# Kernel optimization log

Hardware: AMD Instinct MI355X
Metric: run time of the kernel (lower is better)

Reference implementation:

```python
import jax, jax.numpy as jnp
import numpy as np

B, S_IMG, S_TXT, D, H, HD = 1, 2048, 512, 3072, 24, 128
EMB, N_IP = 4096, 64
IP_SCALE = 1.0
EPS = 1e-6
SM_SCALE = 1.0 / np.sqrt(HD).astype(np.float32)


def _lin(x, W, b=None):
    # torch Linear: y = x @ W.T + b, W: [out, in]
    y = jnp.einsum('bsd,od->bso', x, W)
    return y if b is None else y + b


def _heads(x):  # [B,S,D] -> [B,H,S,HD]
    return x.reshape(B, -1, H, HD).transpose(0, 2, 1, 3)


def _rms(x, w):
    return x * jax.lax.rsqrt(jnp.mean(x * x, axis=-1, keepdims=True) + EPS) * w


def _rope(x, cos, sin):
    # interleaved real/imag rotation, cos/sin: [S, HD] broadcast over B,H
    xr = x.reshape(*x.shape[:-1], HD // 2, 2)
    rot = jnp.stack([-xr[..., 1], xr[..., 0]], axis=-1).reshape(x.shape)
    return x * cos + rot * sin


def _sdpa(q, k, v):
    s = jnp.einsum('bhqd,bhkd->bhqk', q, k) * SM_SCALE
    p = jax.nn.softmax(s, axis=-1)
    return jnp.einsum('bhqk,bhkd->bhqd', p, v)


def setup_inputs() -> dict:
    key = jax.random.key(0)
    ks = jax.random.split(key, 32)
    r = lambda i, shape: jax.random.normal(ks[i], shape, dtype=jnp.float32)
    w = lambda i, shape: r(i, shape) * 0.02
    inp = {
        'hidden_states': r(0, (B, S_IMG, D)),
        'encoder_hidden_states': r(1, (B, S_TXT, D)),
        'image_embeds': r(2, (B, N_IP, EMB)),
        'rope_cos': jnp.cos(r(3, (S_TXT + S_IMG, HD))),
        'rope_sin': jnp.sin(r(3, (S_TXT + S_IMG, HD))),
        'Wq': w(4, (D, D)), 'bq': jnp.zeros((D,)),
        'Wk': w(5, (D, D)), 'bk': jnp.zeros((D,)),
        'Wv': w(6, (D, D)), 'bv': jnp.zeros((D,)),
        'Waq': w(7, (D, D)), 'baq': jnp.zeros((D,)),
        'Wak': w(8, (D, D)), 'bak': jnp.zeros((D,)),
        'Wav': w(9, (D, D)), 'bav': jnp.zeros((D,)),
        'Wo': w(10, (D, D)), 'bo': jnp.zeros((D,)),
        'Wao': w(11, (D, D)), 'bao': jnp.zeros((D,)),
        'norm_q_w': jnp.ones((HD,)), 'norm_k_w': jnp.ones((HD,)),
        'norm_aq_w': jnp.ones((HD,)), 'norm_ak_w': jnp.ones((HD,)),
        'Wk_ip': w(12, (D, EMB)), 'Wv_ip': w(13, (D, EMB)),
        'txt_seq_len': S_TXT,
    }
    return inp


def reference(hidden_states, encoder_hidden_states, image_embeds, rope_cos, rope_sin,
              Wq, bq, Wk, bk, Wv, bv, Waq, baq, Wak, bak, Wav, bav,
              Wo, bo, Wao, bao, norm_q_w, norm_k_w, norm_aq_w, norm_ak_w,
              Wk_ip, Wv_ip, txt_seq_len):
    # main stream projections + per-head RMSNorm
    q = _rms(_heads(_lin(hidden_states, Wq, bq)), norm_q_w)
    k = _rms(_heads(_lin(hidden_states, Wk, bk)), norm_k_w)
    v = _heads(_lin(hidden_states, Wv, bv))
    # encoder (text) stream projections + RMSNorm, concat text before image
    eq = _rms(_heads(_lin(encoder_hidden_states, Waq, baq)), norm_aq_w)
    ek = _rms(_heads(_lin(encoder_hidden_states, Wak, bak)), norm_ak_w)
    ev = _heads(_lin(encoder_hidden_states, Wav, bav))
    q = jnp.concatenate([eq, q], axis=2)
    k = jnp.concatenate([ek, k], axis=2)
    v = jnp.concatenate([ev, v], axis=2)
    # IP-adapter branch uses pre-RoPE image-token queries
    ip_q = q[:, :, txt_seq_len:]
    ip_k = _heads(_lin(image_embeds, Wk_ip))
    ip_v = _heads(_lin(image_embeds, Wv_ip))
    ip_hs = _sdpa(ip_q, ip_k, ip_v).transpose(0, 2, 1, 3).reshape(B, -1, H * HD)
    # rotary on joint q/k, then main attention
    q = _rope(q, rope_cos, rope_sin)
    k = _rope(k, rope_cos, rope_sin)
    hs = _sdpa(q, k, v).transpose(0, 2, 1, 3).reshape(B, -1, H * HD)
    # add scaled IP-adapter output to the image part
    img = hs[:, txt_seq_len:] + IP_SCALE * ip_hs
    enc = hs[:, :txt_seq_len]
    # output projections
    out_img = _lin(img, Wo, bo)
    out_enc = _lin(enc, Wao, bao)
    return out_img, out_enc
```

## Files before the change

kernel.cpp:

```cpp
#include <hip/hip_runtime.h>
#include <hip/hip_bf16.h>

#define H 24
#define HD 128
#define DMODEL 3072
#define S_IMG 2048
#define S_TXT 512
#define S_ALL 2560
#define EMB 4096
#define N_IP 64
#define SM_SCALE 0.08838834764831845f

typedef __attribute__((ext_vector_type(8))) short short8;
typedef __attribute__((ext_vector_type(4))) float f32x4;
typedef __attribute__((ext_vector_type(16))) float f32x16;

__device__ inline unsigned short f2bf(float f) {
    unsigned u = __builtin_bit_cast(unsigned, f);
    return (unsigned short)((u + 0x7fffu + ((u >> 16) & 1u)) >> 16);
}
__device__ inline unsigned pk2(float a, float b) {
    return (unsigned)f2bf(a) | ((unsigned)f2bf(b) << 16);
}
__device__ inline float bf2f(unsigned short u) {
    unsigned x = ((unsigned)u) << 16;
    return __builtin_bit_cast(float, x);
}

__device__ inline void gload16(const void* g, void* l) {
    __builtin_amdgcn_global_load_lds(
        (const __attribute__((address_space(1))) unsigned int*)g,
        (__attribute__((address_space(3))) unsigned int*)(unsigned int)(unsigned long long)l,
        16, 0, 0);
}

struct CastSegs {
    const float* src[13];
    unsigned short* dst[13];
    int n8[13];
    int ntot8[13];
    int bstart[14];
};

__global__ __launch_bounds__(256)
void castall(CastSegs cs)
{
    int b = blockIdx.x, seg = 0;
    while (seg < 12 && b >= cs.bstart[seg + 1]) seg++;
    int nb = cs.bstart[seg + 1] - cs.bstart[seg];
    int lb = b - cs.bstart[seg];
    const float* in = cs.src[seg];
    unsigned short* out = cs.dst[seg];
    int n8 = cs.n8[seg], ntot = cs.ntot8[seg];
    for (int i = lb * 256 + threadIdx.x; i < ntot; i += nb * 256) {
        int4 o;
        if (i < n8) {
            const float4* p = (const float4*)(in + (size_t)i * 8);
            float4 a = p[0], bb = p[1];
            o.x = pk2(a.x, a.y); o.y = pk2(a.z, a.w);
            o.z = pk2(bb.x, bb.y); o.w = pk2(bb.z, bb.w);
        } else {
            o.x = 0; o.y = 0; o.z = 0; o.w = 0;
        }
        *(int4*)(out + (size_t)i * 8) = o;
    }
}

__global__ __launch_bounds__(256)
void bcat2(const float* __restrict__ q0, const float* __restrict__ k0, const float* __restrict__ v0,
           const float* __restrict__ q1, const float* __restrict__ k1, const float* __restrict__ v1,
           float* __restrict__ d0, float* __restrict__ d1)
{
    int i = blockIdx.x * 256 + threadIdx.x;
    int which = i >= 3 * DMODEL;
    int j = which ? i - 3 * DMODEL : i;
    const float* a = which ? q1 : q0;
    const float* b = which ? k1 : k0;
    const float* c = which ? v1 : v0;
    float v = (j < DMODEL) ? a[j] : ((j < 2 * DMODEL) ? b[j - DMODEL] : c[j - 2 * DMODEL]);
    (which ? d1 : d0)[j] = v;
}

struct GSet {
    const unsigned short* A;
    const unsigned short* B;
    const float* bias;
    void* C;
    int N, K, nbn;
};

template<int OUTBF>
__global__ __launch_bounds__(512, 4)
void gemm8(GSet s0, GSet s1, GSet s2, int e0, int e1, int e2,
           const float* cs0, unsigned short* cd0,
           const float* cs1, unsigned short* cd1, int cn8)
{
    __shared__ char sm[73728];
    const int tid = threadIdx.x, lane = tid & 63, wid = tid >> 6;
    const int wm = wid >> 1, wn = wid & 1;
    const int r15 = lane & 15, g = lane >> 4;

    int nwg = gridDim.x;
    int t0 = (blockIdx.x & 7) * (nwg >> 3) + (blockIdx.x >> 3);

    if (t0 >= e2) {
        int lb = t0 - e2;
        const float* src = (lb >> 6) ? cs1 : cs0;
        unsigned short* dst = (lb >> 6) ? cd1 : cd0;
        int b = lb & 63;
        for (int i = b * 512 + tid; i < cn8; i += 64 * 512) {
            const float4* p = (const float4*)(src + (size_t)i * 8);
            float4 a = p[0], bb = p[1];
            int4 o;
            o.x = pk2(a.x, a.y); o.y = pk2(a.z, a.w);
            o.z = pk2(bb.x, bb.y); o.w = pk2(bb.z, bb.w);
            *(int4*)(dst + (size_t)i * 8) = o;
        }
        return;
    }

    GSet S; int local;
    if (t0 < e0)      { S = s0; local = t0; }
    else if (t0 < e1) { S = s1; local = t0 - e0; }
    else              { S = s2; local = t0 - e1; }
    const int mb = local / S.nbn, nb = local - mb * S.nbn;
    const int m0 = mb * 256, n0 = nb * 128;
    const int K = S.K, N = S.N;
    const unsigned short* A = S.A;
    const unsigned short* B = S.B;
    const float* bias = S.bias;

    const int fA0 = tid, fA1 = 512 + tid;
    const int rA0 = fA0 >> 2, sA0 = fA0 & 3;
    const int rA1 = fA1 >> 2, sA1 = fA1 & 3;
    const int rB = tid >> 2, sB = tid & 3;
    const unsigned short* Asrc0 = A + (size_t)(m0 + rA0) * K + ((sA0 ^ ((rA0 >> 1) & 3)) << 3);
    const unsigned short* Asrc1 = A + (size_t)(m0 + rA1) * K + ((sA1 ^ ((rA1 >> 1) & 3)) << 3);
    const unsigned short* Bsrc  = B + (size_t)(n0 + rB) * K + ((sB ^ ((rB >> 1) & 3)) << 3);

    f32x4 acc[4][4];
    #pragma unroll
    for (int i = 0; i < 4; i++)
        #pragma unroll
        for (int j = 0; j < 4; j++)
            acc[i][j] = {0.f, 0.f, 0.f, 0.f};

    const int nt = K >> 5;

    auto STAGE = [&](int buf, int kt) {
        char* d = sm + buf * 24576;
        gload16(Asrc0 + (kt << 5), d + fA0 * 16);
        gload16(Asrc1 + (kt << 5), d + fA1 * 16);
        gload16(Bsrc  + (kt << 5), d + 16384 + tid * 16);
    };

    STAGE(0, 0);
    STAGE(1, 1);
    asm volatile("s_waitcnt vmcnt(3)" ::: "memory");
    __builtin_amdgcn_s_barrier();

    int cur = 0, nxt = 2;
    for (int t = 0; t < nt; t++) {
        if (t + 2 < nt) STAGE(nxt, t + 2);
        const char* As = sm + cur * 24576;
        const char* Bs = As + 16384;
        short8 bfr[4];
        #pragma unroll
        for (int ni = 0; ni < 4; ni++) {
            int brow = wn * 64 + ni * 16 + r15;
            bfr[ni] = *(const short8*)(Bs + brow * 64 + ((g ^ ((brow >> 1) & 3)) << 4));
        }
        __builtin_amdgcn_s_setprio(1);
        #pragma unroll
        for (int mi = 0; mi < 4; mi++) {
            int arow = wm * 64 + mi * 16 + r15;
            short8 af = *(const short8*)(As + arow * 64 + ((g ^ ((arow >> 1) & 3)) << 4));
            #pragma unroll
            for (int ni = 0; ni < 4; ni++)
                acc[mi][ni] = __builtin_amdgcn_mfma_f32_16x16x32_bf16(af, bfr[ni], acc[mi][ni], 0, 0, 0);
        }
        __builtin_amdgcn_s_setprio(0);
        if (t + 1 < nt) {
            if (t + 2 < nt) { asm volatile("s_waitcnt vmcnt(3)" ::: "memory"); }
            else            { asm volatile("s_waitcnt vmcnt(0)" ::: "memory"); }
            __builtin_amdgcn_s_barrier();
        }
        cur = (cur == 2) ? 0 : cur + 1;
        nxt = (nxt == 2) ? 0 : nxt + 1;
    }

    #pragma unroll
    for (int mi = 0; mi < 4; mi++) {
        #pragma unroll
        for (int ni = 0; ni < 4; ni++) {
            int col = n0 + wn * 64 + ni * 16 + r15;
            float bv = bias ? bias[col] : 0.f;
            #pragma unroll
            for (int r = 0; r < 4; r++) {
                int grow = m0 + wm * 64 + mi * 16 + g * 4 + r;
                float v = acc[mi][ni][r] + bv;
                if (OUTBF)
                    ((unsigned short*)S.C)[(size_t)grow * N + col] = f2bf(v);
                else
                    ((float*)S.C)[(size_t)grow * N + col] = v;
            }
        }
    }
}

__device__ inline void vtrans_body(const unsigned short* __restrict__ base, int stride,
                                   unsigned short* __restrict__ vt, int Stot,
                                   int s0, int h, unsigned short* lv, int tid)
{
    const unsigned short* src = base + (size_t)s0 * stride + h * HD;
    #pragma unroll
    for (int i = 0; i < 4; i++) {
        int slot = tid + 256 * i;
        int row = slot >> 4, c = slot & 15;
        int4 v = *(const int4*)(src + (size_t)row * stride + c * 8);
        unsigned* p = (unsigned*)(lv + row * 130 + c * 8);
        p[0] = (unsigned)v.x; p[1] = (unsigned)v.y; p[2] = (unsigned)v.z; p[3] = (unsigned)v.w;
    }
    __syncthreads();
    #pragma unroll
    for (int i = 0; i < 4; i++) {
        int slot = tid + 256 * i;
        int d = slot >> 3, c8 = slot & 7;
        unsigned w0 = lv[(c8 * 8 + 0) * 130 + d] | ((unsigned)lv[(c8 * 8 + 1) * 130 + d] << 16);
        unsigned w1 = lv[(c8 * 8 + 2) * 130 + d] | ((unsigned)lv[(c8 * 8 + 3) * 130 + d] << 16);
        unsigned w2 = lv[(c8 * 8 + 4) * 130 + d] | ((unsigned)lv[(c8 * 8 + 5) * 130 + d] << 16);
        unsigned w3 = lv[(c8 * 8 + 6) * 130 + d] | ((unsigned)lv[(c8 * 8 + 7) * 130 + d] << 16);
        int4 o = {(int)w0, (int)w1, (int)w2, (int)w3};
        *(int4*)(vt + (size_t)(h * HD + d) * Stot + s0 + c8 * 8) = o;
    }
}

__global__ __launch_bounds__(256)
void epilogue(const unsigned short* __restrict__ qkvb, const unsigned short* __restrict__ ipkvb,
              const float* __restrict__ nqw, const float* __restrict__ nkw,
              const float* __restrict__ naqw, const float* __restrict__ nakw,
              const float* __restrict__ cosb, const float* __restrict__ sinb,
              unsigned short* __restrict__ qb, unsigned short* __restrict__ kb,
              unsigned short* __restrict__ ipq,
              unsigned short* __restrict__ vtb, unsigned short* __restrict__ ipkb,
              unsigned short* __restrict__ ipvtb)
{
    __shared__ unsigned short lv[64 * 130];
    const int b = blockIdx.x;
    const int tid = threadIdx.x;

    if (b < 15360) {
        int wg = b * 4 + (tid >> 6);
        int lane = tid & 63;
        int s = wg / H, h = wg - s * H;
        const unsigned short* row = qkvb + (size_t)s * (3 * DMODEL);
        unsigned uq = *(const unsigned*)(row + h * HD + lane * 2);
        unsigned uk = *(const unsigned*)(row + DMODEL + h * HD + lane * 2);
        float q0 = bf2f((unsigned short)uq), q1 = bf2f((unsigned short)(uq >> 16));
        float k0 = bf2f((unsigned short)uk), k1 = bf2f((unsigned short)(uk >> 16));
        float sq = q0 * q0 + q1 * q1, sk = k0 * k0 + k1 * k1;
        #pragma unroll
        for (int off = 1; off < 64; off <<= 1) {
            sq += __shfl_xor(sq, off);
            sk += __shfl_xor(sk, off);
        }
        float rq = rsqrtf(sq * (1.f / HD) + 1e-6f) * SM_SCALE;
        float rk = rsqrtf(sk * (1.f / HD) + 1e-6f);
        const float* wq = (s < S_TXT) ? naqw : nqw;
        const float* wk = (s < S_TXT) ? nakw : nkw;
        float xq0 = q0 * rq * wq[lane * 2], xq1 = q1 * rq * wq[lane * 2 + 1];
        float xk0 = k0 * rk * wk[lane * 2], xk1 = k1 * rk * wk[lane * 2 + 1];
        if (s >= S_TXT)
            *(unsigned*)(ipq + (size_t)h * S_IMG * HD + (size_t)(s - S_TXT) * HD + lane * 2) = pk2(xq0, xq1);
        float c0 = cosb[s * HD + lane * 2], c1 = cosb[s * HD + lane * 2 + 1];
        float s0 = sinb[s * HD + lane * 2], s1 = sinb[s * HD + lane * 2 + 1];
        *(unsigned*)(qb + (size_t)h * S_ALL * HD + (size_t)s * HD + lane * 2) =
            pk2(xq0 * c0 - xq1 * s0, xq1 * c1 + xq0 * s1);
        *(unsigned*)(kb + (size_t)h * S_ALL * HD + (size_t)s * HD + lane * 2) =
            pk2(xk0 * c0 - xk1 * s0, xk1 * c1 + xk0 * s1);
    } else if (b < 16320) {
        int local = b - 15360;
        int bx = local % 40, h = local / 40;
        vtrans_body(qkvb + 2 * DMODEL, 3 * DMODEL, vtb, S_ALL, bx * 64, h, lv, tid);
    } else if (b < 16416) {
        int idx = (b - 16320) * 256 + tid;
        int s = idx / 384;
        int rem = idx - s * 384;
        int h = rem >> 4, d8 = rem & 15;
        int4 v = *(const int4*)(ipkvb + (size_t)s * (2 * DMODEL) + h * HD + d8 * 8);
        *(int4*)(ipkb + ((size_t)h * N_IP + s) * HD + d8 * 8) = v;
    } else {
        int h = b - 16416;
        vtrans_body(ipkvb + DMODEL, 2 * DMODEL, ipvtb, N_IP, 0, h, lv, tid);
    }
}

template<int MODE, int KVBLK, int NQB>
__global__ __launch_bounds__(512, 2)
void flash4(const unsigned short* __restrict__ Q, const unsigned short* __restrict__ Kb,
            const unsigned short* __restrict__ Vt, const unsigned short* __restrict__ ipb,
            unsigned short* __restrict__ Out, int Sq, int Skv)
{
    __shared__ char sm[66560];
    int bid = blockIdx.x;
    int gidx = (bid & 7) * (gridDim.x >> 3) + (bid >> 3);
    const int h = gidx / NQB;
    const int q0 = (gidx - h * NQB) * 256;
    const int tid = threadIdx.x, w = tid >> 6, lane = tid & 63;
    const int l31 = lane & 31, hi = lane >> 5;
    const int T2 = KVBLK / 32, K4 = KVBLK / 16, SLOTV = KVBLK / 8, NL = KVBLK / 32;
    const int VROWB = KVBLK * 2;

    const unsigned short* Qh = Q + ((size_t)h * Sq + q0 + w * 32 + l31) * HD + hi * 8;
    short8 qf[8];
    #pragma unroll
    for (int c = 0; c < 8; c++)
        qf[c] = *(const short8*)(Qh + c * 16);

    float m = -3.0e38f, lsum = 0.f;
    f32x16 o[4];
    #pragma unroll
    for (int dn = 0; dn < 4; dn++)
        #pragma unroll
        for (int r = 0; r < 16; r++) o[dn][r] = 0.f;

    const unsigned short* Kh = Kb + (size_t)h * Skv * HD;
    const unsigned short* Vth = Vt + (size_t)h * HD * Skv;
    float* scl = (float*)(sm + 65536) + w * 32;
    const int nt = Skv / KVBLK;

    for (int t = 0; t < nt; t++) {
        int kv0 = t * KVBLK;
        #pragma unroll
        for (int cc = 0; cc < NL; cc++) {
            int f = cc * 512 + tid;
            int row = f >> 4, slot = f & 15;
            gload16(Kh + (size_t)(kv0 + row) * HD + (((slot * 16) ^ ((row & 7) << 4)) >> 1),
                    sm + f * 16);
        }
        #pragma unroll
        for (int cc = 0; cc < NL; cc++) {
            int f = cc * 512 + tid;
            int d = f / SLOTV, slot = f % SLOTV;
            gload16(Vth + (size_t)d * Skv + kv0 + (((slot * 16) ^ ((d & 7) << 4)) >> 1),
                    sm + 32768 + f * 16);
        }
        __syncthreads();

        f32x16 st[T2];
        __builtin_amdgcn_s_setprio(1);
        #pragma unroll
        for (int t2 = 0; t2 < T2; t2++) {
            #pragma unroll
            for (int r = 0; r < 16; r++) st[t2][r] = 0.f;
            #pragma unroll
            for (int c = 0; c < 8; c++) {
                int krow = t2 * 32 + l31;
                short8 kf = *(const short8*)(sm + krow * 256 + ((c * 32 + hi * 16) ^ ((krow & 7) << 4)));
                st[t2] = __builtin_amdgcn_mfma_f32_32x32x16_bf16(kf, qf[c], st[t2], 0, 0, 0);
            }
        }
        __builtin_amdgcn_s_setprio(0);

        float pmax = st[0][0];
        #pragma unroll
        for (int t2 = 0; t2 < T2; t2++)
            #pragma unroll
            for (int r = 0; r < 16; r++) pmax = fmaxf(pmax, st[t2][r]);
        pmax = fmaxf(pmax, __shfl_xor(pmax, 32));

        if (!__all(pmax - m <= 8.0f)) {
            float mn = fmaxf(m, pmax);
            float sc = __expf(m - mn);
            m = mn;
            lsum *= sc;
            if (hi == 0) scl[l31] = sc;
            float scb[16];
            #pragma unroll
            for (int r = 0; r < 16; r++)
                scb[r] = scl[(r & 3) + 8 * (r >> 2) + 4 * hi];
            #pragma unroll
            for (int dn = 0; dn < 4; dn++)
                #pragma unroll
                for (int r = 0; r < 16; r++) o[dn][r] *= scb[r];
        }

        float psum = 0.f;
        #pragma unroll
        for (int t2 = 0; t2 < T2; t2++)
            #pragma unroll
            for (int r = 0; r < 16; r++) {
                float p = __expf(st[t2][r] - m);
                st[t2][r] = p;
                psum += p;
            }
        psum += __shfl_xor(psum, 32);
        lsum += psum;

        short8 pa[K4];
        #pragma unroll
        for (int k4 = 0; k4 < K4; k4++) {
            unsigned U  = pk2(st[(k4 * 8 + 0) >> 4][(k4 * 8 + 0) & 15], st[(k4 * 8 + 1) >> 4][(k4 * 8 + 1) & 15]);
            unsigned V  = pk2(st[(k4 * 8 + 2) >> 4][(k4 * 8 + 2) & 15], st[(k4 * 8 + 3) >> 4][(k4 * 8 + 3) & 15]);
            unsigned U2 = pk2(st[(k4 * 8 + 4) >> 4][(k4 * 8 + 4) & 15], st[(k4 * 8 + 5) >> 4][(k4 * 8 + 5) & 15]);
            unsigned V2 = pk2(st[(k4 * 8 + 6) >> 4][(k4 * 8 + 6) & 15], st[(k4 * 8 + 7) >> 4][(k4 * 8 + 7) & 15]);
            unsigned SU = __shfl_xor(U, 32), SU2 = __shfl_xor(U2, 32);
            unsigned SV = __shfl_xor(V, 32), SV2 = __shfl_xor(V2, 32);
            uint4 wv;
            wv.x = hi ? SU2 : U;
            wv.y = hi ? SV2 : V;
            wv.z = hi ? U2 : SU;
            wv.w = hi ? V2 : SV;
            pa[k4] = __builtin_bit_cast(short8, wv);
        }

        __builtin_amdgcn_s_setprio(1);
        #pragma unroll
        for (int dn = 0; dn < 4; dn++) {
            #pragma unroll
            for (int k4 = 0; k4 < K4; k4++) {
                int vrow = dn * 32 + l31;
                short8 vf = *(const short8*)(sm + 32768 + vrow * VROWB + ((k4 * 32 + hi * 16) ^ ((vrow & 7) << 4)));
                o[dn] = __builtin_amdgcn_mfma_f32_32x32x16_bf16(pa[k4], vf, o[dn], 0, 0, 0);
            }
        }
        __builtin_amdgcn_s_setprio(0);
        __syncthreads();
    }

    if (hi == 0) scl[l31] = 1.f / lsum;
    float linv[16];
    #pragma unroll
    for (int r = 0; r < 16; r++)
        linv[r] = scl[(r & 3) + 8 * (r >> 2) + 4 * hi];
    #pragma unroll
    for (int dn = 0; dn < 4; dn++) {
        #pragma unroll
        for (int r = 0; r < 16; r++) {
            int qrow = q0 + w * 32 + (r & 3) + 8 * (r >> 2) + 4 * hi;
            int col = h * HD + dn * 32 + l31;
            float val = o[dn][r] * linv[r];
            if (MODE == 1 && qrow >= S_TXT)
                val += bf2f(ipb[(size_t)(qrow - S_TXT) * DMODEL + col]);
            Out[(size_t)qrow * DMODEL + col] = f2bf(val);
        }
    }
}

extern "C" void kernel_launch(void* const* d_in, const int* in_sizes, int n_in,
                              void* d_out, int out_size, void* d_ws, size_t ws_size,
                              hipStream_t stream)
{
    const float* hs   = (const float*)d_in[0];
    const float* enc  = (const float*)d_in[1];
    const float* iemb = (const float*)d_in[2];
    const float* cosb = (const float*)d_in[3];
    const float* sinb = (const float*)d_in[4];
    const float* Wq  = (const float*)d_in[5];  const float* bq  = (const float*)d_in[6];
    const float* Wk  = (const float*)d_in[7];  const float* bk  = (const float*)d_in[8];
    const float* Wv  = (const float*)d_in[9];  const float* bv  = (const float*)d_in[10];
    const float* Waq = (const float*)d_in[11]; const float* baq = (const float*)d_in[12];
    const float* Wak = (const float*)d_in[13]; const float* bak = (const float*)d_in[14];
    const float* Wav = (const float*)d_in[15]; const float* bav = (const float*)d_in[16];
    const float* Wo  = (const float*)d_in[17]; const float* bo  = (const float*)d_in[18];
    const float* Wao = (const float*)d_in[19]; const float* bao = (const float*)d_in[20];
    const float* nq  = (const float*)d_in[21]; const float* nk  = (const float*)d_in[22];
    const float* naq = (const float*)d_in[23]; const float* nak = (const float*)d_in[24];
    const float* Wkip = (const float*)d_in[25]; const float* Wvip = (const float*)d_in[26];
    (void)in_sizes; (void)n_in; (void)out_size; (void)ws_size;

    char* ws = (char*)d_ws;
    size_t off = 0;
    auto alloc = [&](size_t b) { char* p = ws + off; off += (b + 255) & ~(size_t)255; return p; };
    unsigned short* qkvb    = (unsigned short*)alloc((size_t)S_ALL * 3 * DMODEL * 2);
    unsigned short* ipkvb   = (unsigned short*)alloc((size_t)256 * 2 * DMODEL * 2);
    unsigned short* hs_bf   = (unsigned short*)alloc((size_t)S_IMG * DMODEL * 2);
    unsigned short* enc_bf  = (unsigned short*)alloc((size_t)S_TXT * DMODEL * 2);
    unsigned short* iemb_bf = (unsigned short*)alloc((size_t)256 * EMB * 2);
    unsigned short* Wqkv  = (unsigned short*)alloc((size_t)3 * DMODEL * DMODEL * 2);
    unsigned short* Waqkv = (unsigned short*)alloc((size_t)3 * DMODEL * DMODEL * 2);
    unsigned short* Wo_b  = (unsigned short*)alloc((size_t)DMODEL * DMODEL * 2);
    unsigned short* Wao_b = (unsigned short*)alloc((size_t)DMODEL * DMODEL * 2);
    unsigned short* Wip   = (unsigned short*)alloc((size_t)2 * DMODEL * EMB * 2);
    float* bqkv  = (float*)alloc(3 * DMODEL * 4);
    float* baqkv = (float*)alloc(3 * DMODEL * 4);
    unsigned short* qb    = (unsigned short*)alloc((size_t)H * S_ALL * HD * 2);
    unsigned short* kbf   = (unsigned short*)alloc((size_t)H * S_ALL * HD * 2);
    unsigned short* vtb   = (unsigned short*)alloc((size_t)H * HD * S_ALL * 2);
    unsigned short* ipqb  = (unsigned short*)alloc((size_t)H * S_IMG * HD * 2);
    unsigned short* ipkb  = (unsigned short*)alloc((size_t)H * N_IP * HD * 2);
    unsigned short* ipvtb = (unsigned short*)alloc((size_t)H * HD * N_IP * 2);
    unsigned short* ipbuf = (unsigned short*)alloc((size_t)S_IMG * DMODEL * 2);
    unsigned short* attnb = (unsigned short*)alloc((size_t)S_ALL * DMODEL * 2);

    const size_t DD = (size_t)DMODEL * DMODEL;
    const size_t DE = (size_t)DMODEL * EMB;
    const int D8 = (int)(DD / 8), E8 = (int)(DE / 8);

    CastSegs cs;
    const float* srcs[11] = {hs, enc, iemb, Wq, Wk, Wv, Waq, Wak, Wav, Wkip, Wvip};
    unsigned short* dsts[11] = {hs_bf, enc_bf, iemb_bf,
                                Wqkv, Wqkv + DD, Wqkv + 2 * DD,
                                Waqkv, Waqkv + DD, Waqkv + 2 * DD,
                                Wip, Wip + DE};
    int n8s[11]  = {S_IMG * DMODEL / 8, S_TXT * DMODEL / 8, N_IP * EMB / 8,
                    D8, D8, D8, D8, D8, D8, E8, E8};
    int nt8s[11] = {S_IMG * DMODEL / 8, S_TXT * DMODEL / 8, 256 * EMB / 8,
                    D8, D8, D8, D8, D8, D8, E8, E8};
    int acc = 0;
    for (int i = 0; i < 11; i++) {
        cs.src[i] = srcs[i]; cs.dst[i] = dsts[i];
        cs.n8[i] = n8s[i]; cs.ntot8[i] = nt8s[i];
        cs.bstart[i] = acc;
        int nb = (nt8s[i] + 8191) / 8192;
        acc += (nb < 1 ? 1 : nb);
    }
    for (int i = 11; i < 14; i++) cs.bstart[i] = acc;

    dim3 blk(256);
    castall<<<dim3(acc), blk, 0, stream>>>(cs);
    bcat2<<<dim3(72), blk, 0, stream>>>(bq, bk, bv, baq, bak, bav, bqkv, baqkv);

    GSet sIp  = {iemb_bf, Wip,  nullptr, ipkvb,                           2 * DMODEL, EMB,    48};
    GSet sImg = {hs_bf,  Wqkv,  bqkv,  qkvb + (size_t)S_TXT * 3 * DMODEL, 3 * DMODEL, DMODEL, 72};
    GSet sTxt = {enc_bf, Waqkv, baqkv, qkvb,                              3 * DMODEL, DMODEL, 72};
    gemm8<1><<<dim3(896), dim3(512), 0, stream>>>(
        sIp, sImg, sTxt, 48, 624, 768,
        Wo, Wo_b, Wao, Wao_b, D8);

    epilogue<<<dim3(16440), blk, 0, stream>>>(
        qkvb, ipkvb, nq, nk, naq, nak, cosb, sinb,
        qb, kbf, ipqb, vtb, ipkb, ipvtb);

    dim3 fblk(512);
    flash4<0, 64, 8><<<dim3(192), fblk, 0, stream>>>(ipqb, ipkb, ipvtb, nullptr, ipbuf, S_IMG, N_IP);
    flash4<1, 128, 10><<<dim3(240), fblk, 0, stream>>>(qb, kbf, vtb, ipbuf, attnb, S_ALL, S_ALL);

    GSet oImg = {attnb + (size_t)S_TXT * DMODEL, Wo_b,  bo,  d_out,                                DMODEL, DMODEL, 24};
    GSet oTxt = {attnb,                          Wao_b, bao, (float*)d_out + (size_t)S_IMG * DMODEL, DMODEL, DMODEL, 24};
    gemm8<0><<<dim3(240), dim3(512), 0, stream>>>(
        oImg, oTxt, oTxt, 192, 240, 240,
        nullptr, nullptr, nullptr, nullptr, 0);
}
```

Before: 553.9 us.

## Split main attention KV range in two and merge partials in combine kernel

Main flash attention now splits the KV range into two halves, doubling the block count so more CUs are occupied. Each split writes unnormalized-by-global fp32 partial outputs plus per-row max and sum, and a new combine kernel merges them with log-sum-exp weights and adds the IP-adapter output. This adds a large fp32 round trip through memory and an extra launch, and reuses consumed weight buffers as scratch.

Measured after the change: 565.3 us. +2.1%, slower.

```diff
diff --git a/kernel.cpp b/kernel.cpp
--- a/kernel.cpp
+++ b/kernel.cpp
@@ -295,17 +295,28 @@
     }
 }
 
-template<int MODE, int KVBLK, int NQB>
+template<int MODE, int KVBLK, int NQB, int NSPLIT>
 __global__ __launch_bounds__(512, 2)
-void flash4(const unsigned short* __restrict__ Q, const unsigned short* __restrict__ Kb,
-            const unsigned short* __restrict__ Vt, const unsigned short* __restrict__ ipb,
-            unsigned short* __restrict__ Out, int Sq, int Skv)
+void flash5(const unsigned short* __restrict__ Q, const unsigned short* __restrict__ Kb,
+            const unsigned short* __restrict__ Vt, unsigned short* __restrict__ Out,
+            float* __restrict__ opart, float* __restrict__ ml, int Sq, int Skv)
 {
     __shared__ char sm[66560];
     int bid = blockIdx.x;
     int gidx = (bid & 7) * (gridDim.x >> 3) + (bid >> 3);
-    const int h = gidx / NQB;
-    const int q0 = (gidx - h * NQB) * 256;
+    int h, q0, split, tstart, tend;
+    if (NSPLIT == 1) {
+        h = gidx / NQB;
+        q0 = (gidx - h * NQB) * 256;
+        split = 0; tstart = 0; tend = Skv / KVBLK;
+    } else {
+        h = gidx / (NQB * NSPLIT);
+        int r2 = gidx - h * (NQB * NSPLIT);
+        split = r2 / NQB;
+        q0 = (r2 - split * NQB) * 256;
+        int ntt = Skv / KVBLK / NSPLIT;
+        tstart = split * ntt; tend = tstart + ntt;
+    }
     const int tid = threadIdx.x, w = tid >> 6, lane = tid & 63;
     const int l31 = lane & 31, hi = lane >> 5;
     const int T2 = KVBLK / 32, K4 = KVBLK / 16, SLOTV = KVBLK / 8, NL = KVBLK / 32;
@@ -327,9 +338,8 @@
     const unsigned short* Kh = Kb + (size_t)h * Skv * HD;
     const unsigned short* Vth = Vt + (size_t)h * HD * Skv;
     float* scl = (float*)(sm + 65536) + w * 32;
-    const int nt = Skv / KVBLK;
-
-    for (int t = 0; t < nt; t++) {
+
+    for (int t = tstart; t < tend; t++) {
         int kv0 = t * KVBLK;
         #pragma unroll
         for (int cc = 0; cc < NL; cc++) {
@@ -440,11 +450,56 @@
             int qrow = q0 + w * 32 + (r & 3) + 8 * (r >> 2) + 4 * hi;
             int col = h * HD + dn * 32 + l31;
             float val = o[dn][r] * linv[r];
-            if (MODE == 1 && qrow >= S_TXT)
-                val += bf2f(ipb[(size_t)(qrow - S_TXT) * DMODEL + col]);
-            Out[(size_t)qrow * DMODEL + col] = f2bf(val);
-        }
-    }
+            if (MODE == 0)
+                Out[(size_t)qrow * DMODEL + col] = f2bf(val);
+            else
+                opart[((size_t)split * S_ALL + qrow) * DMODEL + col] = val;
+        }
+    }
+    if (MODE == 2 && hi == 0) {
+        int q = q0 + w * 32 + l31;
+        size_t mi_ = ((size_t)(split * H + h) * S_ALL + q) * 2;
+        ml[mi_] = m;
+        ml[mi_ + 1] = lsum;
+    }
+}
+
+__global__ __launch_bounds__(256)
+void combine2(const float* __restrict__ opart, const float* __restrict__ ml,
+              const unsigned short* __restrict__ ipb, unsigned short* __restrict__ outb)
+{
+    int idx = blockIdx.x * 256 + threadIdx.x;
+    int qrow = idx / 384;
+    int c8 = idx - qrow * 384;
+    int col = c8 * 8;
+    int h = col >> 7;
+    size_t b0 = ((size_t)(0 * H + h) * S_ALL + qrow) * 2;
+    size_t b1 = ((size_t)(1 * H + h) * S_ALL + qrow) * 2;
+    float m0 = ml[b0], l0 = ml[b0 + 1];
+    float m1 = ml[b1], l1 = ml[b1 + 1];
+    float M = fmaxf(m0, m1);
+    float w0 = l0 * __expf(m0 - M), w1 = l1 * __expf(m1 - M);
+    float inv = 1.f / (w0 + w1);
+    w0 *= inv; w1 *= inv;
+    const float* p0 = opart + ((size_t)0 * S_ALL + qrow) * DMODEL + col;
+    const float* p1 = opart + ((size_t)1 * S_ALL + qrow) * DMODEL + col;
+    float4 a0 = *(const float4*)p0, a1 = *(const float4*)(p0 + 4);
+    float4 c0 = *(const float4*)p1, c1 = *(const float4*)(p1 + 4);
+    float v[8];
+    v[0] = w0 * a0.x + w1 * c0.x; v[1] = w0 * a0.y + w1 * c0.y;
+    v[2] = w0 * a0.z + w1 * c0.z; v[3] = w0 * a0.w + w1 * c0.w;
+    v[4] = w0 * a1.x + w1 * c1.x; v[5] = w0 * a1.y + w1 * c1.y;
+    v[6] = w0 * a1.z + w1 * c1.z; v[7] = w0 * a1.w + w1 * c1.w;
+    if (qrow >= S_TXT) {
+        int4 ipv = *(const int4*)(ipb + (size_t)(qrow - S_TXT) * DMODEL + col);
+        const unsigned short* ip = (const unsigned short*)&ipv;
+        #pragma unroll
+        for (int j = 0; j < 8; j++) v[j] += bf2f(ip[j]);
+    }
+    int4 o;
+    o.x = pk2(v[0], v[1]); o.y = pk2(v[2], v[3]);
+    o.z = pk2(v[4], v[5]); o.w = pk2(v[6], v[7]);
+    *(int4*)(outb + (size_t)qrow * DMODEL + col) = o;
 }
 
 extern "C" void kernel_launch(void* const* d_in, const int* in_sizes, int n_in,
@@ -493,6 +548,9 @@
     unsigned short* ipbuf = (unsigned short*)alloc((size_t)S_IMG * DMODEL * 2);
     unsigned short* attnb = (unsigned short*)alloc((size_t)S_ALL * DMODEL * 2);
 
+    float* opart = (float*)Wqkv;
+    float* mlbuf = (float*)Wip;
+
     const size_t DD = (size_t)DMODEL * DMODEL;
     const size_t DE = (size_t)DMODEL * EMB;
     const int D8 = (int)(DD / 8), E8 = (int)(DE / 8);
@@ -533,8 +591,11 @@
         qb, kbf, ipqb, vtb, ipkb, ipvtb);
 
     dim3 fblk(512);
-    flash4<0, 64, 8><<<dim3(192), fblk, 0, stream>>>(ipqb, ipkb, ipvtb, nullptr, ipbuf, S_IMG, N_IP);
-    flash4<1, 128, 10><<<dim3(240), fblk, 0, stream>>>(qb, kbf, vtb, ipbuf, attnb, S_ALL, S_ALL);
+    flash5<0, 64, 8, 1><<<dim3(192), fblk, 0, stream>>>(
+        ipqb, ipkb, ipvtb, ipbuf, nullptr, nullptr, S_IMG, N_IP);
+    flash5<2, 128, 10, 2><<<dim3(480), fblk, 0, stream>>>(
+        qb, kbf, vtb, nullptr, opart, mlbuf, S_ALL, S_ALL);
+    combine2<<<dim3(3840), blk, 0, stream>>>(opart, mlbuf, ipbuf, attnb);
 
     GSet oImg = {attnb + (size_t)S_TXT * DMODEL, Wo_b,  bo,  d_out,                                DMODEL, DMODEL, 24};
     GSet oTxt = {attnb,                          Wao_b, bao, (float*)d_out + (size_t)S_IMG * DMODEL, DMODEL, DMODEL, 24};
```
